# Kernel optimization log

Hardware: AMD Instinct MI355X
Metric: run time of the kernel (lower is better)

Reference implementation:

```python
import jax, jax.numpy as jnp
import numpy as np

N_NODES = 50000
N_EDGES = 800000
N_GRAPHS = 128
IN, HID, OUT, CLS = 128, 128, 128, 10


def setup_inputs() -> dict:
    key = jax.random.key(0)
    ks = jax.random.split(key, 16)
    d = {}
    d["features"] = jax.random.normal(ks[0], (N_NODES, IN), jnp.float32)
    d["edge_src"] = jax.random.randint(ks[1], (N_EDGES,), 0, N_NODES)
    d["edge_dst"] = jax.random.randint(ks[2], (N_EDGES,), 0, N_NODES)
    d["graph_ids"] = jnp.sort(jax.random.randint(ks[3], (N_NODES,), 0, N_GRAPHS))

    def lin(k, i, o):
        return (jax.random.normal(k, (i, o), jnp.float32) / np.float32(np.sqrt(i)))

    dims = [(IN, HID), (HID, HID), (HID, OUT)]
    for l, (i, o) in enumerate(dims):
        d[f"Ws{l}"] = lin(ks[4 + 3 * l], i, o)
        d[f"Wn{l}"] = lin(ks[5 + 3 * l], i, o)
        d[f"b{l}"] = jnp.zeros((o,), jnp.float32)
    d["Wf"] = lin(ks[13], OUT, CLS)
    d["bf"] = jnp.zeros((CLS,), jnp.float32)
    return d


def _sage_mean_layer(h, edge_src, edge_dst, Ws, Wn, b, in_deg):
    # mean-aggregate in-neighbor features: gather at src, segment-sum at dst
    msg_sum = jax.ops.segment_sum(h[edge_src], edge_dst, num_segments=N_NODES)
    h_neigh = msg_sum / in_deg  # [N, d], zero-degree nodes divide by 1 -> 0
    return jax.nn.relu(h @ Ws + h_neigh @ Wn + b)


def reference(features, edge_src, edge_dst, graph_ids,
              Ws0, Wn0, b0, Ws1, Wn1, b1, Ws2, Wn2, b2, Wf, bf):
    ones = jnp.ones((N_EDGES,), jnp.float32)
    in_deg = jax.ops.segment_sum(ones, edge_dst, num_segments=N_NODES)
    in_deg = jnp.maximum(in_deg, 1.0)[:, None]  # [N, 1]

    h = features
    h = _sage_mean_layer(h, edge_src, edge_dst, Ws0, Wn0, b0, in_deg)
    h = _sage_mean_layer(h, edge_src, edge_dst, Ws1, Wn1, b1, in_deg)
    h = _sage_mean_layer(h, edge_src, edge_dst, Ws2, Wn2, b2, in_deg)

    # mean graph pooling over node segments
    node_ones = jnp.ones((N_NODES,), jnp.float32)
    counts = jax.ops.segment_sum(node_ones, graph_ids, num_segments=N_GRAPHS)
    counts = jnp.maximum(counts, 1.0)[:, None]
    pooled = jax.ops.segment_sum(h, graph_ids, num_segments=N_GRAPHS) / counts

    return pooled @ Wf + bf  # [N_GRAPHS, CLS]
```

## Files before the change

### kernel.cpp

```cpp
#include <hip/hip_runtime.h>

#define N_NODES  50000
#define N_EDGES  800000
#define N_GRAPHS 128
#define HD       128
#define K2       256
#define CLS      10
#define NPART    8
#define PSIZE    (N_NODES / NPART)
#define NSUB     16
#define NB_SCAN  ((N_NODES + 255) / 256)
#define NBIN     1600
#define CHUNK    (N_EDGES / NBIN)
#define PCAP     131072
#define NSLOT    16

typedef __attribute__((ext_vector_type(8))) _Float16 f16x8;
typedef __attribute__((ext_vector_type(4))) float f32x4;
typedef __attribute__((ext_vector_type(2))) float f32x2;

union U4H8 { uint4 u; _Float16 h[8]; };
union U2H4 { uint2 u; _Float16 h[4]; };

typedef const __attribute__((address_space(1))) void* gptr_t;
typedef __attribute__((address_space(3))) void* lptr_t;
#define GLOAD_LDS16(g, l) \
    __builtin_amdgcn_global_load_lds((gptr_t)(g), (lptr_t)(l), 16, 0, 0)

__global__ __launch_bounds__(512) void k_zero(int* __restrict__ z) {
    int i = threadIdx.x;
    if (i < 264) z[i] = 0;
}

__global__ __launch_bounds__(256) void k_bin(const int* __restrict__ src, const int* __restrict__ dst,
                                             unsigned* __restrict__ stag, int* __restrict__ gcount) {
    __shared__ int lcount[NPART];
    __shared__ int lbase[NPART];
    const int tid = threadIdx.x;
    const int lo = blockIdx.x * CHUNK;
    if (tid < NPART) lcount[tid] = 0;
    __syncthreads();
    int dc[2], sc[2];
#pragma unroll
    for (int it = 0; it < 2; ++it) {
        int i = lo + tid + it * 256;
        dc[it] = -1;
        if (i < lo + CHUNK) {
            int d = dst[i];
            dc[it] = d; sc[it] = src[i];
            atomicAdd(&lcount[d / PSIZE], 1);
        }
    }
    __syncthreads();
    if (tid < NPART) {
        lbase[tid] = atomicAdd(&gcount[tid], lcount[tid]);
        lcount[tid] = 0;
    }
    __syncthreads();
#pragma unroll
    for (int it = 0; it < 2; ++it) {
        if (dc[it] >= 0) {
            int p = dc[it] / PSIZE;
            int slot = atomicAdd(&lcount[p], 1);
            stag[(size_t)p * PCAP + lbase[p] + slot] =
                (unsigned)sc[it] | ((unsigned)(dc[it] - p * PSIZE) << 16);
        }
    }
}

__global__ __launch_bounds__(512) void k_hist(const unsigned* __restrict__ stag,
                                              const int* __restrict__ gcount,
                                              int* __restrict__ ghist) {
    __shared__ int hist[PSIZE];
    const int tid = threadIdx.x;
    const int p = blockIdx.x & (NPART - 1);
    const int s = blockIdx.x >> 3;
    for (int j = tid; j < PSIZE; j += 512) hist[j] = 0;
    __syncthreads();
    const int n = gcount[p];
    const int cs = (int)(((long long)s * n) / NSUB);
    const int ce = (int)(((long long)(s + 1) * n) / NSUB);
    const unsigned* sp = stag + (size_t)p * PCAP;
    for (int i = cs + tid; i < ce; i += 512)
        atomicAdd(&hist[sp[i] >> 16], 1);
    __syncthreads();
    int* gh = ghist + (size_t)blockIdx.x * PSIZE;
    for (int j = tid; j < PSIZE; j += 512) gh[j] = hist[j];
}

__global__ __launch_bounds__(256) void k_scan(int* __restrict__ ghist,
                                              int* __restrict__ rowptr,
                                              int* __restrict__ bsum, int* __restrict__ bflag) {
    __shared__ int sc[256];
    __shared__ int r[256];
    const int tid = threadIdx.x;
    const int b = blockIdx.x;
    const int node = b * 256 + tid;
    int d[NSUB];
    int deg = 0, p = 0, off = 0;
    if (node < N_NODES) {
        p = node / PSIZE; off = node - p * PSIZE;
#pragma unroll
        for (int s = 0; s < NSUB; ++s) {
            d[s] = ghist[(size_t)(s * NPART + p) * PSIZE + off];
            deg += d[s];
        }
    }
    sc[tid] = deg;
    __syncthreads();
    for (int o = 1; o < 256; o <<= 1) {
        int add = (tid >= o) ? sc[tid - o] : 0;
        __syncthreads();
        sc[tid] += add;
        __syncthreads();
    }
    if (tid == 255) {
        __hip_atomic_store(&bsum[b], sc[255], __ATOMIC_RELAXED, __HIP_MEMORY_SCOPE_AGENT);
        __hip_atomic_store(&bflag[b], 1, __ATOMIC_RELEASE, __HIP_MEMORY_SCOPE_AGENT);
    }
    int agg = 0;
    if (tid < b) {
        while (__hip_atomic_load(&bflag[tid], __ATOMIC_ACQUIRE, __HIP_MEMORY_SCOPE_AGENT) == 0) {}
        agg = __hip_atomic_load(&bsum[tid], __ATOMIC_RELAXED, __HIP_MEMORY_SCOPE_AGENT);
    }
    r[tid] = agg;
    __syncthreads();
    for (int o = 128; o > 0; o >>= 1) {
        if (tid < o) r[tid] += r[tid + o];
        __syncthreads();
    }
    if (node < N_NODES) {
        int base = r[0] + sc[tid] - deg;
        rowptr[node] = base;
        int c = base;
#pragma unroll
        for (int s = 0; s < NSUB; ++s) {
            ghist[(size_t)(s * NPART + p) * PSIZE + off] = c;
            c += d[s];
        }
    }
    if (b == NB_SCAN - 1 && tid == 0) rowptr[N_NODES] = N_EDGES;
}

#define INIT_ITEMS (800000 + 3 * HD * K2 + N_GRAPHS * HD + N_GRAPHS)
#define INIT_BLOCKS5 ((INIT_ITEMS + 511) / 512)
__global__ __launch_bounds__(512) void k_scatterinit(
    const unsigned* __restrict__ stag, const int* __restrict__ gcount,
    const int* __restrict__ ghist, int* __restrict__ eidx,
    const float* __restrict__ f, unsigned short* __restrict__ c0, unsigned char* __restrict__ f8,
    const float* __restrict__ Ws0, const float* __restrict__ Wn0,
    const float* __restrict__ Ws1, const float* __restrict__ Wn1,
    const float* __restrict__ Ws2, const float* __restrict__ Wn2,
    unsigned short* __restrict__ wt, float* __restrict__ pooled,
    const int* __restrict__ gid, float* __restrict__ counts) {
    if (blockIdx.x < 128) {
        __shared__ int cur[PSIZE];
        const int tid = threadIdx.x;
        const int p = blockIdx.x & (NPART - 1);
        const int s = blockIdx.x >> 3;
        const int* gh = ghist + (size_t)blockIdx.x * PSIZE;
        for (int j = tid; j < PSIZE; j += 512) cur[j] = gh[j];
        __syncthreads();
        const int n = gcount[p];
        const int cs = (int)(((long long)s * n) / NSUB);
        const int ce = (int)(((long long)(s + 1) * n) / NSUB);
        const unsigned* sp = stag + (size_t)p * PCAP;
        for (int i = cs + tid; i < ce; i += 512) {
            unsigned v = sp[i];
            int slot = atomicAdd(&cur[v >> 16], 1);
            eidx[slot] = (int)(v & 0xFFFFu);
        }
        return;
    }
    long long gi = (long long)(blockIdx.x - 128) * 512 + threadIdx.x;
    if (gi < 800000) {
        int t = (int)gi;
        int row = t >> 4, c8 = (t & 15) * 8;
        const float* p = f + (size_t)row * HD + c8;
        float4 a = *(const float4*)p;
        float4 b = *(const float4*)(p + 4);
        U4H8 v;
        v.h[0] = (_Float16)a.x; v.h[1] = (_Float16)a.y;
        v.h[2] = (_Float16)a.z; v.h[3] = (_Float16)a.w;
        v.h[4] = (_Float16)b.x; v.h[5] = (_Float16)b.y;
        v.h[6] = (_Float16)b.z; v.h[7] = (_Float16)b.w;
        *(uint4*)(c0 + (size_t)row * K2 + c8) = v.u;
        int p0 = __builtin_amdgcn_cvt_pk_fp8_f32(a.x, a.y, 0, false);
        p0 = __builtin_amdgcn_cvt_pk_fp8_f32(a.z, a.w, p0, true);
        int p1 = __builtin_amdgcn_cvt_pk_fp8_f32(b.x, b.y, 0, false);
        p1 = __builtin_amdgcn_cvt_pk_fp8_f32(b.z, b.w, p1, true);
        *(uint2*)(f8 + (size_t)row * HD + c8) = make_uint2((unsigned)p0, (unsigned)p1);
        return;
    }
    gi -= 800000;
    if (gi < 3 * HD * K2) {
        int t = (int)gi;
        int l = t / (HD * K2), r = t % (HD * K2);
        int n = r / K2, k = r % K2;
        const float* Ws = (l == 0) ? Ws0 : (l == 1) ? Ws1 : Ws2;
        const float* Wn = (l == 0) ? Wn0 : (l == 1) ? Wn1 : Wn2;
        float w = (k < HD) ? Ws[k * HD + n] : Wn[(k - HD) * HD + n];
        union { unsigned short u; _Float16 h; } c;
        c.h = (_Float16)w;
        wt[t] = c.u;
        return;
    }
    gi -= 3 * HD * K2;
    if (gi < N_GRAPHS * HD) { pooled[gi] = 0.f; return; }
    gi -= (long long)N_GRAPHS * HD;
    if (gi < N_GRAPHS) {
        int g = (int)gi;
        int lo = 0, hi = N_NODES;
        while (lo < hi) { int mid = (lo + hi) >> 1; if (gid[mid] < g) lo = mid + 1; else hi = mid; }
        int start = lo;
        lo = 0; hi = N_NODES;
        while (lo < hi) { int mid = (lo + hi) >> 1; if (gid[mid] <= g) lo = mid + 1; else hi = mid; }
        counts[g] = (float)(lo - start);
    }
}

__global__ __launch_bounds__(256) void k_gather(const unsigned char* __restrict__ h8,
                                                const int* __restrict__ rowptr,
                                                const int* __restrict__ eidx,
                                                unsigned short* __restrict__ msg) {
    const int node = (blockIdx.x * 256 + threadIdx.x) >> 6;
    const int lane = threadIdx.x & 63;
    if (node >= N_NODES) return;
    const int epar = lane >> 4;
    const int d0 = (lane & 15) * 8;
    const int beg = rowptr[node], end = rowptr[node + 1];
    float acc[8] = {0.f, 0.f, 0.f, 0.f, 0.f, 0.f, 0.f, 0.f};
    int j = beg + epar;
    for (; j + 12 < end; j += 16) {
        int s0 = eidx[j], s1 = eidx[j + 4], s2 = eidx[j + 8], s3 = eidx[j + 12];
        uint2 v0 = *(const uint2*)(h8 + (size_t)s0 * HD + d0);
        uint2 v1 = *(const uint2*)(h8 + (size_t)s1 * HD + d0);
        uint2 v2 = *(const uint2*)(h8 + (size_t)s2 * HD + d0);
        uint2 v3 = *(const uint2*)(h8 + (size_t)s3 * HD + d0);
        f32x2 e;
        e = __builtin_amdgcn_cvt_pk_f32_fp8(v0.x, false); acc[0] += e[0]; acc[1] += e[1];
        e = __builtin_amdgcn_cvt_pk_f32_fp8(v0.x, true);  acc[2] += e[0]; acc[3] += e[1];
        e = __builtin_amdgcn_cvt_pk_f32_fp8(v0.y, false); acc[4] += e[0]; acc[5] += e[1];
        e = __builtin_amdgcn_cvt_pk_f32_fp8(v0.y, true);  acc[6] += e[0]; acc[7] += e[1];
        e = __builtin_amdgcn_cvt_pk_f32_fp8(v1.x, false); acc[0] += e[0]; acc[1] += e[1];
        e = __builtin_amdgcn_cvt_pk_f32_fp8(v1.x, true);  acc[2] += e[0]; acc[3] += e[1];
        e = __builtin_amdgcn_cvt_pk_f32_fp8(v1.y, false); acc[4] += e[0]; acc[5] += e[1];
        e = __builtin_amdgcn_cvt_pk_f32_fp8(v1.y, true);  acc[6] += e[0]; acc[7] += e[1];
        e = __builtin_amdgcn_cvt_pk_f32_fp8(v2.x, false); acc[0] += e[0]; acc[1] += e[1];
        e = __builtin_amdgcn_cvt_pk_f32_fp8(v2.x, true);  acc[2] += e[0]; acc[3] += e[1];
        e = __builtin_amdgcn_cvt_pk_f32_fp8(v2.y, false); acc[4] += e[0]; acc[5] += e[1];
        e = __builtin_amdgcn_cvt_pk_f32_fp8(v2.y, true);  acc[6] += e[0]; acc[7] += e[1];
        e = __builtin_amdgcn_cvt_pk_f32_fp8(v3.x, false); acc[0] += e[0]; acc[1] += e[1];
        e = __builtin_amdgcn_cvt_pk_f32_fp8(v3.x, true);  acc[2] += e[0]; acc[3] += e[1];
        e = __builtin_amdgcn_cvt_pk_f32_fp8(v3.y, false); acc[4] += e[0]; acc[5] += e[1];
        e = __builtin_amdgcn_cvt_pk_f32_fp8(v3.y, true);  acc[6] += e[0]; acc[7] += e[1];
    }
    for (; j < end; j += 4) {
        uint2 v0 = *(const uint2*)(h8 + (size_t)eidx[j] * HD + d0);
        f32x2 e;
        e = __builtin_amdgcn_cvt_pk_f32_fp8(v0.x, false); acc[0] += e[0]; acc[1] += e[1];
        e = __builtin_amdgcn_cvt_pk_f32_fp8(v0.x, true);  acc[2] += e[0]; acc[3] += e[1];
        e = __builtin_amdgcn_cvt_pk_f32_fp8(v0.y, false); acc[4] += e[0]; acc[5] += e[1];
        e = __builtin_amdgcn_cvt_pk_f32_fp8(v0.y, true);  acc[6] += e[0]; acc[7] += e[1];
    }
#pragma unroll
    for (int i = 0; i < 8; ++i) {
        acc[i] += __shfl_xor(acc[i], 16);
        acc[i] += __shfl_xor(acc[i], 32);
    }
    if (epar == 0) {
        float inv = (end > beg) ? 1.0f / (float)(end - beg) : 0.f;
        U4H8 o;
#pragma unroll
        for (int i = 0; i < 8; ++i) o.h[i] = (_Float16)(acc[i] * inv);
        *(uint4*)(msg + (size_t)node * K2 + HD + d0) = o.u;
    }
}

__global__ __launch_bounds__(256) void k_sage(const unsigned short* __restrict__ hin,
                                              const unsigned short* __restrict__ wt,
                                              const float* __restrict__ bias,
                                              unsigned short* __restrict__ hout,
                                              unsigned char* __restrict__ hout8,
                                              const int* __restrict__ gid,
                                              float* __restrict__ pooled,
                                              int write16, int dopool) {
    __shared__ __align__(16) _Float16 Ah[2][128 * 64];
    __shared__ __align__(16) _Float16 Bw[2][128 * 64];
    __shared__ float gpool[NSLOT][HD];
    __shared__ int ginfo[2];
    const int tid = threadIdx.x;
    const int wv = tid >> 6, lane = tid & 63;
    const int m0 = blockIdx.x * 128;
    const int m_off = (wv >> 1) * 64, n_off = (wv & 1) * 64;
    const int l15 = lane & 15, q = lane >> 4;

    f32x4 acc[4][4];
#pragma unroll
    for (int a = 0; a < 4; ++a)
#pragma unroll
        for (int b = 0; b < 4; ++b) acc[a][b] = (f32x4){0.f, 0.f, 0.f, 0.f};

    auto stage = [&](int bsel, int kt) {
        const int k0 = kt * 64;
#pragma unroll
        for (int i = 0; i < 4; ++i) {
            int idx = tid + i * 256;
            int row = idx >> 3, c = idx & 7;
            int qs = (c ^ (row & 7)) * 8;
            int gm = m0 + row;
            if (gm < N_NODES)
                GLOAD_LDS16(hin + (size_t)gm * K2 + k0 + qs, &Ah[bsel][idx * 8]);
            GLOAD_LDS16(wt + (size_t)row * K2 + k0 + qs, &Bw[bsel][idx * 8]);
        }
    };

    stage(0, 0);
    __syncthreads();
#pragma unroll
    for (int kt = 0; kt < 4; ++kt) {
        const int b = kt & 1;
        if (kt < 3) stage(b ^ 1, kt + 1);
        f16x8 hf[4][2], wf[4][2];
#pragma unroll
        for (int mt = 0; mt < 4; ++mt) {
            const int row = m_off + mt * 16 + l15;
            const int sw = row & 7;
#pragma unroll
            for (int ks = 0; ks < 2; ++ks)
                hf[mt][ks] = *(const f16x8*)&Ah[b][row * 64 + (((ks * 4 + q) ^ sw) * 8)];
        }
#pragma unroll
        for (int nt = 0; nt < 4; ++nt) {
            const int row = n_off + nt * 16 + l15;
            const int sw = row & 7;
#pragma unroll
            for (int ks = 0; ks < 2; ++ks)
                wf[nt][ks] = *(const f16x8*)&Bw[b][row * 64 + (((ks * 4 + q) ^ sw) * 8)];
        }
#pragma unroll
        for (int mt = 0; mt < 4; ++mt)
#pragma unroll
            for (int nt = 0; nt < 4; ++nt) {
                acc[mt][nt] = __builtin_amdgcn_mfma_f32_16x16x32_f16(wf[nt][0], hf[mt][0], acc[mt][nt], 0, 0, 0);
                acc[mt][nt] = __builtin_amdgcn_mfma_f32_16x16x32_f16(wf[nt][1], hf[mt][1], acc[mt][nt], 0, 0, 0);
            }
        __syncthreads();
    }
    if (!dopool) {
#pragma unroll
        for (int nt = 0; nt < 4; ++nt) {
            int n = n_off + nt * 16 + q * 4;
            float4 bv = *(const float4*)(bias + n);
#pragma unroll
            for (int mt = 0; mt < 4; ++mt) {
                int m = m0 + m_off + mt * 16 + l15;
                if (m < N_NODES) {
                    f32x4 a = acc[mt][nt];
                    float r0 = fmaxf(a[0] + bv.x, 0.f);
                    float r1 = fmaxf(a[1] + bv.y, 0.f);
                    float r2 = fmaxf(a[2] + bv.z, 0.f);
                    float r3 = fmaxf(a[3] + bv.w, 0.f);
                    if (write16) {
                        U2H4 v;
                        v.h[0] = (_Float16)r0; v.h[1] = (_Float16)r1;
                        v.h[2] = (_Float16)r2; v.h[3] = (_Float16)r3;
                        *(uint2*)(hout + (size_t)m * K2 + n) = v.u;
                    }
                    int p = __builtin_amdgcn_cvt_pk_fp8_f32(r0, r1, 0, false);
                    p = __builtin_amdgcn_cvt_pk_fp8_f32(r2, r3, p, true);
                    *(unsigned int*)(hout8 + (size_t)m * HD + n) = (unsigned)p;
                }
            }
        }
    } else {
        for (int j = tid; j < NSLOT * HD; j += 256) ((float*)gpool)[j] = 0.f;
        if (tid == 0) {
            ginfo[0] = gid[m0];
            ginfo[1] = gid[min(m0 + 127, N_NODES - 1)];
        }
        __syncthreads();
        const int g_lo = ginfo[0];
        int gg[4];
#pragma unroll
        for (int mt = 0; mt < 4; ++mt) {
            int m = m0 + m_off + mt * 16 + l15;
            gg[mt] = (m < N_NODES) ? gid[m] : -1;
        }
#pragma unroll
        for (int nt = 0; nt < 4; ++nt) {
            int n = n_off + nt * 16 + q * 4;
            float4 bv = *(const float4*)(bias + n);
            int cur = -1;
            float p0 = 0.f, p1 = 0.f, p2 = 0.f, p3 = 0.f;
#pragma unroll
            for (int mt = 0; mt < 4; ++mt) {
                if (gg[mt] < 0) continue;
                f32x4 a = acc[mt][nt];
                float r0 = fmaxf(a[0] + bv.x, 0.f);
                float r1 = fmaxf(a[1] + bv.y, 0.f);
                float r2 = fmaxf(a[2] + bv.z, 0.f);
                float r3 = fmaxf(a[3] + bv.w, 0.f);
                if (gg[mt] != cur) {
                    if (cur >= 0) {
                        int s = cur - g_lo;
                        if (s < NSLOT) {
                            atomicAdd(&gpool[s][n], p0); atomicAdd(&gpool[s][n + 1], p1);
                            atomicAdd(&gpool[s][n + 2], p2); atomicAdd(&gpool[s][n + 3], p3);
                        } else {
                            atomicAdd(&pooled[(size_t)cur * HD + n], p0);
                            atomicAdd(&pooled[(size_t)cur * HD + n + 1], p1);
                            atomicAdd(&pooled[(size_t)cur * HD + n + 2], p2);
                            atomicAdd(&pooled[(size_t)cur * HD + n + 3], p3);
                        }
                    }
                    cur = gg[mt]; p0 = r0; p1 = r1; p2 = r2; p3 = r3;
                } else {
                    p0 += r0; p1 += r1; p2 += r2; p3 += r3;
                }
            }
            if (cur >= 0) {
                int s = cur - g_lo;
                if (s < NSLOT) {
                    atomicAdd(&gpool[s][n], p0); atomicAdd(&gpool[s][n + 1], p1);
                    atomicAdd(&gpool[s][n + 2], p2); atomicAdd(&gpool[s][n + 3], p3);
                } else {
                    atomicAdd(&pooled[(size_t)cur * HD + n], p0);
                    atomicAdd(&pooled[(size_t)cur * HD + n + 1], p1);
                    atomicAdd(&pooled[(size_t)cur * HD + n + 2], p2);
                    atomicAdd(&pooled[(size_t)cur * HD + n + 3], p3);
                }
            }
        }
        __syncthreads();
        const int nslot = min(NSLOT, ginfo[1] - g_lo + 1);
        for (int j = tid; j < nslot * HD; j += 256) {
            float v = gpool[j >> 7][j & 127];
            if (v != 0.f)
                atomicAdd(&pooled[(size_t)(g_lo + (j >> 7)) * HD + (j & 127)], v);
        }
    }
}

__global__ __launch_bounds__(256) void k_final(const float* __restrict__ pooled,
                                               const float* __restrict__ counts,
                                               const float* __restrict__ Wf,
                                               const float* __restrict__ bf,
                                               float* __restrict__ out) {
    int t = blockIdx.x * 256 + threadIdx.x;
    if (t >= N_GRAPHS * CLS) return;
    int g = t / CLS, c = t % CLS;
    float inv = 1.0f / fmaxf(counts[g], 1.0f);
    float s = 0.f;
    for (int k = 0; k < HD; ++k) s += pooled[(size_t)g * HD + k] * Wf[k * CLS + c];
    out[t] = s * inv + bf[c];
}

extern "C" void kernel_launch(void* const* d_in, const int* in_sizes, int n_in,
                              void* d_out, int out_size, void* d_ws, size_t ws_size,
                              hipStream_t stream) {
    const float* features = (const float*)d_in[0];
    const int*   esrc     = (const int*)d_in[1];
    const int*   edst     = (const int*)d_in[2];
    const int*   gids     = (const int*)d_in[3];
    const float* bs[3]  = {(const float*)d_in[6], (const float*)d_in[9], (const float*)d_in[12]};
    const float* Wf = (const float*)d_in[13];
    const float* bfv = (const float*)d_in[14];
    float* out = (float*)d_out;

    int* gcount = (int*)d_ws;
    int* bflag  = gcount + 8;
    int* bsum   = bflag + 256;
    int* rowptr = bsum + 256;
    int* eidx   = rowptr + 50008;
    unsigned* stag = (unsigned*)(eidx + 800000);
    int* ghist  = (int*)(stag + (size_t)NPART * PCAP);
    float* pooled = (float*)(ghist + (size_t)NPART * NSUB * PSIZE);
    float* counts = pooled + N_GRAPHS * HD;
    unsigned short* C0 = (unsigned short*)(counts + 128);
    unsigned short* C1 = C0 + (size_t)N_NODES * K2;
    unsigned short* C2 = C1 + (size_t)N_NODES * K2;
    unsigned short* Wt = C2 + (size_t)N_NODES * K2;
    unsigned char* F0 = (unsigned char*)(Wt + 3 * HD * K2);
    unsigned char* F1 = F0 + (size_t)N_NODES * HD;
    unsigned char* F2 = F1 + (size_t)N_NODES * HD;

    k_zero<<<1, 512, 0, stream>>>(gcount);

    k_bin<<<NBIN, 256, 0, stream>>>(esrc, edst, stag, gcount);
    k_hist<<<NPART * NSUB, 512, 0, stream>>>(stag, gcount, ghist);
    k_scan<<<NB_SCAN, 256, 0, stream>>>(ghist, rowptr, bsum, bflag);
    k_scatterinit<<<128 + INIT_BLOCKS5, 512, 0, stream>>>(
        stag, gcount, ghist, eidx,
        features, C0, F0,
        (const float*)d_in[4], (const float*)d_in[5],
        (const float*)d_in[7], (const float*)d_in[8],
        (const float*)d_in[10], (const float*)d_in[11],
        Wt, pooled, gids, counts);

    unsigned short* C[4] = {C0, C1, C2, C0};
    unsigned char* F[4] = {F0, F1, F2, F0};
    for (int l = 0; l < 3; ++l) {
        k_gather<<<(N_NODES * 64 + 255) / 256, 256, 0, stream>>>(F[l], rowptr, eidx, C[l]);
        k_sage<<<(N_NODES + 127) / 128, 256, 0, stream>>>(
            C[l], Wt + (size_t)l * HD * K2, bs[l], C[l + 1], F[l + 1],
            gids, pooled, (l < 2) ? 1 : 0, (l == 2) ? 1 : 0);
    }

    k_final<<<(N_GRAPHS * CLS + 255) / 256, 256, 0, stream>>>(pooled, counts, Wf, bfv, out);
}
```

Before: 291.5 us.

## Fuse neighbor gather into SAGE GEMM kernel with LDS-resident messages

Merges the per-layer gather kernel and the GEMM kernel into one 512-thread kernel. Each block first aggregates the mean neighbor messages for its 128 nodes into shared memory, then runs the MFMA GEMM reading the self half from global and the neighbor half from LDS. This removes the global write and re-read of the message half of the concatenated buffer and one launch per layer, and it narrows the activation buffers to 128 columns. In exchange the gather parallelism per block is serialized over 16 nodes per wave, double buffering is replaced by single-buffer staging with extra barriers, and LDS use grows, which may lower occupancy.

```diff
diff --git a/kernel.cpp b/kernel.cpp
--- a/kernel.cpp
+++ b/kernel.cpp
@@ -184,7 +184,7 @@
         v.h[2] = (_Float16)a.z; v.h[3] = (_Float16)a.w;
         v.h[4] = (_Float16)b.x; v.h[5] = (_Float16)b.y;
         v.h[6] = (_Float16)b.z; v.h[7] = (_Float16)b.w;
-        *(uint4*)(c0 + (size_t)row * K2 + c8) = v.u;
+        *(uint4*)(c0 + (size_t)row * HD + c8) = v.u;
         int p0 = __builtin_amdgcn_cvt_pk_fp8_f32(a.x, a.y, 0, false);
         p0 = __builtin_amdgcn_cvt_pk_fp8_f32(a.z, a.w, p0, true);
         int p1 = __builtin_amdgcn_cvt_pk_fp8_f32(b.x, b.y, 0, false);
@@ -219,116 +219,130 @@
     }
 }
 
-__global__ __launch_bounds__(256) void k_gather(const unsigned char* __restrict__ h8,
-                                                const int* __restrict__ rowptr,
-                                                const int* __restrict__ eidx,
-                                                unsigned short* __restrict__ msg) {
-    const int node = (blockIdx.x * 256 + threadIdx.x) >> 6;
-    const int lane = threadIdx.x & 63;
-    if (node >= N_NODES) return;
-    const int epar = lane >> 4;
-    const int d0 = (lane & 15) * 8;
-    const int beg = rowptr[node], end = rowptr[node + 1];
-    float acc[8] = {0.f, 0.f, 0.f, 0.f, 0.f, 0.f, 0.f, 0.f};
-    int j = beg + epar;
-    for (; j + 12 < end; j += 16) {
-        int s0 = eidx[j], s1 = eidx[j + 4], s2 = eidx[j + 8], s3 = eidx[j + 12];
-        uint2 v0 = *(const uint2*)(h8 + (size_t)s0 * HD + d0);
-        uint2 v1 = *(const uint2*)(h8 + (size_t)s1 * HD + d0);
-        uint2 v2 = *(const uint2*)(h8 + (size_t)s2 * HD + d0);
-        uint2 v3 = *(const uint2*)(h8 + (size_t)s3 * HD + d0);
-        f32x2 e;
-        e = __builtin_amdgcn_cvt_pk_f32_fp8(v0.x, false); acc[0] += e[0]; acc[1] += e[1];
-        e = __builtin_amdgcn_cvt_pk_f32_fp8(v0.x, true);  acc[2] += e[0]; acc[3] += e[1];
-        e = __builtin_amdgcn_cvt_pk_f32_fp8(v0.y, false); acc[4] += e[0]; acc[5] += e[1];
-        e = __builtin_amdgcn_cvt_pk_f32_fp8(v0.y, true);  acc[6] += e[0]; acc[7] += e[1];
-        e = __builtin_amdgcn_cvt_pk_f32_fp8(v1.x, false); acc[0] += e[0]; acc[1] += e[1];
-        e = __builtin_amdgcn_cvt_pk_f32_fp8(v1.x, true);  acc[2] += e[0]; acc[3] += e[1];
-        e = __builtin_amdgcn_cvt_pk_f32_fp8(v1.y, false); acc[4] += e[0]; acc[5] += e[1];
-        e = __builtin_amdgcn_cvt_pk_f32_fp8(v1.y, true);  acc[6] += e[0]; acc[7] += e[1];
-        e = __builtin_amdgcn_cvt_pk_f32_fp8(v2.x, false); acc[0] += e[0]; acc[1] += e[1];
-        e = __builtin_amdgcn_cvt_pk_f32_fp8(v2.x, true);  acc[2] += e[0]; acc[3] += e[1];
-        e = __builtin_amdgcn_cvt_pk_f32_fp8(v2.y, false); acc[4] += e[0]; acc[5] += e[1];
-        e = __builtin_amdgcn_cvt_pk_f32_fp8(v2.y, true);  acc[6] += e[0]; acc[7] += e[1];
-        e = __builtin_amdgcn_cvt_pk_f32_fp8(v3.x, false); acc[0] += e[0]; acc[1] += e[1];
-        e = __builtin_amdgcn_cvt_pk_f32_fp8(v3.x, true);  acc[2] += e[0]; acc[3] += e[1];
-        e = __builtin_amdgcn_cvt_pk_f32_fp8(v3.y, false); acc[4] += e[0]; acc[5] += e[1];
-        e = __builtin_amdgcn_cvt_pk_f32_fp8(v3.y, true);  acc[6] += e[0]; acc[7] += e[1];
-    }
-    for (; j < end; j += 4) {
-        uint2 v0 = *(const uint2*)(h8 + (size_t)eidx[j] * HD + d0);
-        f32x2 e;
-        e = __builtin_amdgcn_cvt_pk_f32_fp8(v0.x, false); acc[0] += e[0]; acc[1] += e[1];
-        e = __builtin_amdgcn_cvt_pk_f32_fp8(v0.x, true);  acc[2] += e[0]; acc[3] += e[1];
-        e = __builtin_amdgcn_cvt_pk_f32_fp8(v0.y, false); acc[4] += e[0]; acc[5] += e[1];
-        e = __builtin_amdgcn_cvt_pk_f32_fp8(v0.y, true);  acc[6] += e[0]; acc[7] += e[1];
-    }
-#pragma unroll
-    for (int i = 0; i < 8; ++i) {
-        acc[i] += __shfl_xor(acc[i], 16);
-        acc[i] += __shfl_xor(acc[i], 32);
-    }
-    if (epar == 0) {
-        float inv = (end > beg) ? 1.0f / (float)(end - beg) : 0.f;
-        U4H8 o;
-#pragma unroll
-        for (int i = 0; i < 8; ++i) o.h[i] = (_Float16)(acc[i] * inv);
-        *(uint4*)(msg + (size_t)node * K2 + HD + d0) = o.u;
-    }
-}
-
-__global__ __launch_bounds__(256) void k_sage(const unsigned short* __restrict__ hin,
-                                              const unsigned short* __restrict__ wt,
-                                              const float* __restrict__ bias,
-                                              unsigned short* __restrict__ hout,
-                                              unsigned char* __restrict__ hout8,
-                                              const int* __restrict__ gid,
-                                              float* __restrict__ pooled,
-                                              int write16, int dopool) {
-    __shared__ __align__(16) _Float16 Ah[2][128 * 64];
-    __shared__ __align__(16) _Float16 Bw[2][128 * 64];
-    __shared__ float gpool[NSLOT][HD];
+__global__ __launch_bounds__(512) void k_gsage(const unsigned char* __restrict__ h8,
+                                               const unsigned short* __restrict__ hin,
+                                               const int* __restrict__ rowptr,
+                                               const int* __restrict__ eidx,
+                                               const unsigned short* __restrict__ wt,
+                                               const float* __restrict__ bias,
+                                               unsigned short* __restrict__ hout,
+                                               unsigned char* __restrict__ hout8,
+                                               const int* __restrict__ gid,
+                                               float* __restrict__ pooled,
+                                               int dopool) {
+    __shared__ __align__(16) char arena[65536];
+    _Float16* Ah  = (_Float16*)arena;
+    _Float16* Bw  = (_Float16*)(arena + 16384);
+    _Float16* msg = (_Float16*)(arena + 32768);
+    float (*gpool)[HD] = (float(*)[HD])arena;
     __shared__ int ginfo[2];
     const int tid = threadIdx.x;
     const int wv = tid >> 6, lane = tid & 63;
     const int m0 = blockIdx.x * 128;
-    const int m_off = (wv >> 1) * 64, n_off = (wv & 1) * 64;
+    const int m_off = (wv >> 1) * 32, n_off = (wv & 1) * 64;
     const int l15 = lane & 15, q = lane >> 4;
 
-    f32x4 acc[4][4];
-#pragma unroll
-    for (int a = 0; a < 4; ++a)
-#pragma unroll
-        for (int b = 0; b < 4; ++b) acc[a][b] = (f32x4){0.f, 0.f, 0.f, 0.f};
-
-    auto stage = [&](int bsel, int kt) {
+    auto stageA = [&](int kt) {
         const int k0 = kt * 64;
 #pragma unroll
-        for (int i = 0; i < 4; ++i) {
-            int idx = tid + i * 256;
+        for (int i = 0; i < 2; ++i) {
+            int idx = tid + i * 512;
             int row = idx >> 3, c = idx & 7;
             int qs = (c ^ (row & 7)) * 8;
             int gm = m0 + row;
             if (gm < N_NODES)
-                GLOAD_LDS16(hin + (size_t)gm * K2 + k0 + qs, &Ah[bsel][idx * 8]);
-            GLOAD_LDS16(wt + (size_t)row * K2 + k0 + qs, &Bw[bsel][idx * 8]);
+                GLOAD_LDS16(hin + (size_t)gm * HD + k0 + qs, &Ah[idx * 8]);
         }
     };
-
-    stage(0, 0);
-    __syncthreads();
+    auto stageB = [&](int kt) {
+        const int k0 = kt * 64;
+#pragma unroll
+        for (int i = 0; i < 2; ++i) {
+            int idx = tid + i * 512;
+            int row = idx >> 3, c = idx & 7;
+            int qs = (c ^ (row & 7)) * 8;
+            GLOAD_LDS16(wt + (size_t)row * K2 + k0 + qs, &Bw[idx * 8]);
+        }
+    };
+
+    stageA(0); stageB(0);
+
+    const int epar = lane >> 4;
+    const int d0 = l15 * 8;
+    for (int i = 0; i < 16; ++i) {
+        const int r = wv * 16 + i;
+        const int node = m0 + r;
+        if (node >= N_NODES) break;
+        const int beg = rowptr[node], end = rowptr[node + 1];
+        float acc[8] = {0.f, 0.f, 0.f, 0.f, 0.f, 0.f, 0.f, 0.f};
+        int j = beg + epar;
+        for (; j + 12 < end; j += 16) {
+            int s0 = eidx[j], s1 = eidx[j + 4], s2 = eidx[j + 8], s3 = eidx[j + 12];
+            uint2 v0 = *(const uint2*)(h8 + (size_t)s0 * HD + d0);
+            uint2 v1 = *(const uint2*)(h8 + (size_t)s1 * HD + d0);
+            uint2 v2 = *(const uint2*)(h8 + (size_t)s2 * HD + d0);
+            uint2 v3 = *(const uint2*)(h8 + (size_t)s3 * HD + d0);
+            f32x2 e;
+            e = __builtin_amdgcn_cvt_pk_f32_fp8(v0.x, false); acc[0] += e[0]; acc[1] += e[1];
+            e = __builtin_amdgcn_cvt_pk_f32_fp8(v0.x, true);  acc[2] += e[0]; acc[3] += e[1];
+            e = __builtin_amdgcn_cvt_pk_f32_fp8(v0.y, false); acc[4] += e[0]; acc[5] += e[1];
+            e = __builtin_amdgcn_cvt_pk_f32_fp8(v0.y, true);  acc[6] += e[0]; acc[7] += e[1];
+            e = __builtin_amdgcn_cvt_pk_f32_fp8(v1.x, false); acc[0] += e[0]; acc[1] += e[1];
+            e = __builtin_amdgcn_cvt_pk_f32_fp8(v1.x, true);  acc[2] += e[0]; acc[3] += e[1];
+            e = __builtin_amdgcn_cvt_pk_f32_fp8(v1.y, false); acc[4] += e[0]; acc[5] += e[1];
+            e = __builtin_amdgcn_cvt_pk_f32_fp8(v1.y, true);  acc[6] += e[0]; acc[7] += e[1];
+            e = __builtin_amdgcn_cvt_pk_f32_fp8(v2.x, false); acc[0] += e[0]; acc[1] += e[1];
+            e = __builtin_amdgcn_cvt_pk_f32_fp8(v2.x, true);  acc[2] += e[0]; acc[3] += e[1];
+            e = __builtin_amdgcn_cvt_pk_f32_fp8(v2.y, false); acc[4] += e[0]; acc[5] += e[1];
+            e = __builtin_amdgcn_cvt_pk_f32_fp8(v2.y, true);  acc[6] += e[0]; acc[7] += e[1];
+            e = __builtin_amdgcn_cvt_pk_f32_fp8(v3.x, false); acc[0] += e[0]; acc[1] += e[1];
+            e = __builtin_amdgcn_cvt_pk_f32_fp8(v3.x, true);  acc[2] += e[0]; acc[3] += e[1];
+            e = __builtin_amdgcn_cvt_pk_f32_fp8(v3.y, false); acc[4] += e[0]; acc[5] += e[1];
+            e = __builtin_amdgcn_cvt_pk_f32_fp8(v3.y, true);  acc[6] += e[0]; acc[7] += e[1];
+        }
+        for (; j < end; j += 4) {
+            uint2 v0 = *(const uint2*)(h8 + (size_t)eidx[j] * HD + d0);
+            f32x2 e;
+            e = __builtin_amdgcn_cvt_pk_f32_fp8(v0.x, false); acc[0] += e[0]; acc[1] += e[1];
+            e = __builtin_amdgcn_cvt_pk_f32_fp8(v0.x, true);  acc[2] += e[0]; acc[3] += e[1];
+            e = __builtin_amdgcn_cvt_pk_f32_fp8(v0.y, false); acc[4] += e[0]; acc[5] += e[1];
+            e = __builtin_amdgcn_cvt_pk_f32_fp8(v0.y, true);  acc[6] += e[0]; acc[7] += e[1];
+        }
+#pragma unroll
+        for (int k = 0; k < 8; ++k) {
+            acc[k] += __shfl_xor(acc[k], 16);
+            acc[k] += __shfl_xor(acc[k], 32);
+        }
+        if (epar == 0) {
+            float inv = (end > beg) ? 1.0f / (float)(end - beg) : 0.f;
+            U4H8 o;
+#pragma unroll
+            for (int k = 0; k < 8; ++k) o.h[k] = (_Float16)(acc[k] * inv);
+            *(uint4*)&msg[(size_t)r * 128 + ((l15 ^ (r & 7)) * 8)] = o.u;
+        }
+    }
+    __syncthreads();
+
+    f32x4 acc[2][4];
+#pragma unroll
+    for (int a = 0; a < 2; ++a)
+#pragma unroll
+        for (int b = 0; b < 4; ++b) acc[a][b] = (f32x4){0.f, 0.f, 0.f, 0.f};
+
 #pragma unroll
     for (int kt = 0; kt < 4; ++kt) {
-        const int b = kt & 1;
-        if (kt < 3) stage(b ^ 1, kt + 1);
-        f16x8 hf[4][2], wf[4][2];
-#pragma unroll
-        for (int mt = 0; mt < 4; ++mt) {
+        f16x8 hf[2][2], wf[4][2];
+#pragma unroll
+        for (int mt = 0; mt < 2; ++mt) {
             const int row = m_off + mt * 16 + l15;
             const int sw = row & 7;
 #pragma unroll
-            for (int ks = 0; ks < 2; ++ks)
-                hf[mt][ks] = *(const f16x8*)&Ah[b][row * 64 + (((ks * 4 + q) ^ sw) * 8)];
+            for (int ks = 0; ks < 2; ++ks) {
+                if (kt < 2)
+                    hf[mt][ks] = *(const f16x8*)&Ah[row * 64 + (((ks * 4 + q) ^ sw) * 8)];
+                else
+                    hf[mt][ks] = *(const f16x8*)&msg[row * 128 + ((((kt - 2) * 8 + ks * 4 + q) ^ sw) * 8)];
+            }
         }
 #pragma unroll
         for (int nt = 0; nt < 4; ++nt) {
@@ -336,10 +350,15 @@
             const int sw = row & 7;
 #pragma unroll
             for (int ks = 0; ks < 2; ++ks)
-                wf[nt][ks] = *(const f16x8*)&Bw[b][row * 64 + (((ks * 4 + q) ^ sw) * 8)];
-        }
-#pragma unroll
-        for (int mt = 0; mt < 4; ++mt)
+                wf[nt][ks] = *(const f16x8*)&Bw[row * 64 + (((ks * 4 + q) ^ sw) * 8)];
+        }
+        __syncthreads();
+        if (kt < 3) {
+            if (kt == 0) stageA(1);
+            stageB(kt + 1);
+        }
+#pragma unroll
+        for (int mt = 0; mt < 2; ++mt)
 #pragma unroll
             for (int nt = 0; nt < 4; ++nt) {
                 acc[mt][nt] = __builtin_amdgcn_mfma_f32_16x16x32_f16(wf[nt][0], hf[mt][0], acc[mt][nt], 0, 0, 0);
@@ -347,13 +366,14 @@
             }
         __syncthreads();
     }
+
     if (!dopool) {
 #pragma unroll
         for (int nt = 0; nt < 4; ++nt) {
             int n = n_off + nt * 16 + q * 4;
             float4 bv = *(const float4*)(bias + n);
 #pragma unroll
-            for (int mt = 0; mt < 4; ++mt) {
+            for (int mt = 0; mt < 2; ++mt) {
                 int m = m0 + m_off + mt * 16 + l15;
                 if (m < N_NODES) {
                     f32x4 a = acc[mt][nt];
@@ -361,12 +381,10 @@
                     float r1 = fmaxf(a[1] + bv.y, 0.f);
                     float r2 = fmaxf(a[2] + bv.z, 0.f);
                     float r3 = fmaxf(a[3] + bv.w, 0.f);
-                    if (write16) {
-                        U2H4 v;
-                        v.h[0] = (_Float16)r0; v.h[1] = (_Float16)r1;
-                        v.h[2] = (_Float16)r2; v.h[3] = (_Float16)r3;
-                        *(uint2*)(hout + (size_t)m * K2 + n) = v.u;
-                    }
+                    U2H4 v;
+                    v.h[0] = (_Float16)r0; v.h[1] = (_Float16)r1;
+                    v.h[2] = (_Float16)r2; v.h[3] = (_Float16)r3;
+                    *(uint2*)(hout + (size_t)m * HD + n) = v.u;
                     int p = __builtin_amdgcn_cvt_pk_fp8_f32(r0, r1, 0, false);
                     p = __builtin_amdgcn_cvt_pk_fp8_f32(r2, r3, p, true);
                     *(unsigned int*)(hout8 + (size_t)m * HD + n) = (unsigned)p;
@@ -374,16 +392,16 @@
             }
         }
     } else {
-        for (int j = tid; j < NSLOT * HD; j += 256) ((float*)gpool)[j] = 0.f;
+        for (int j = tid; j < NSLOT * HD; j += 512) ((float*)gpool)[j] = 0.f;
         if (tid == 0) {
             ginfo[0] = gid[m0];
             ginfo[1] = gid[min(m0 + 127, N_NODES - 1)];
         }
         __syncthreads();
         const int g_lo = ginfo[0];
-        int gg[4];
-#pragma unroll
-        for (int mt = 0; mt < 4; ++mt) {
+        int gg[2];
+#pragma unroll
+        for (int mt = 0; mt < 2; ++mt) {
             int m = m0 + m_off + mt * 16 + l15;
             gg[mt] = (m < N_NODES) ? gid[m] : -1;
         }
@@ -394,7 +412,7 @@
             int cur = -1;
             float p0 = 0.f, p1 = 0.f, p2 = 0.f, p3 = 0.f;
 #pragma unroll
-            for (int mt = 0; mt < 4; ++mt) {
+            for (int mt = 0; mt < 2; ++mt) {
                 if (gg[mt] < 0) continue;
                 f32x4 a = acc[mt][nt];
                 float r0 = fmaxf(a[0] + bv.x, 0.f);
@@ -434,7 +452,7 @@
         }
         __syncthreads();
         const int nslot = min(NSLOT, ginfo[1] - g_lo + 1);
-        for (int j = tid; j < nslot * HD; j += 256) {
+        for (int j = tid; j < nslot * HD; j += 512) {
             float v = gpool[j >> 7][j & 127];
             if (v != 0.f)
                 atomicAdd(&pooled[(size_t)(g_lo + (j >> 7)) * HD + (j & 127)], v);
@@ -478,9 +496,9 @@
     float* pooled = (float*)(ghist + (size_t)NPART * NSUB * PSIZE);
     float* counts = pooled + N_GRAPHS * HD;
     unsigned short* C0 = (unsigned short*)(counts + 128);
-    unsigned short* C1 = C0 + (size_t)N_NODES * K2;
-    unsigned short* C2 = C1 + (size_t)N_NODES * K2;
-    unsigned short* Wt = C2 + (size_t)N_NODES * K2;
+    unsigned short* C1 = C0 + (size_t)N_NODES * HD;
+    unsigned short* C2 = C1 + (size_t)N_NODES * HD;
+    unsigned short* Wt = C2 + (size_t)N_NODES * HD;
     unsigned char* F0 = (unsigned char*)(Wt + 3 * HD * K2);
     unsigned char* F1 = F0 + (size_t)N_NODES * HD;
     unsigned char* F2 = F1 + (size_t)N_NODES * HD;
@@ -501,10 +519,9 @@
     unsigned short* C[4] = {C0, C1, C2, C0};
     unsigned char* F[4] = {F0, F1, F2, F0};
     for (int l = 0; l < 3; ++l) {
-        k_gather<<<(N_NODES * 64 + 255) / 256, 256, 0, stream>>>(F[l], rowptr, eidx, C[l]);
-        k_sage<<<(N_NODES + 127) / 128, 256, 0, stream>>>(
-            C[l], Wt + (size_t)l * HD * K2, bs[l], C[l + 1], F[l + 1],
-            gids, pooled, (l < 2) ? 1 : 0, (l == 2) ? 1 : 0);
+        k_gsage<<<(N_NODES + 127) / 128, 512, 0, stream>>>(
+            F[l], C[l], rowptr, eidx, Wt + (size_t)l * HD * K2, bs[l],
+            C[l + 1], F[l + 1], gids, pooled, (l == 2) ? 1 : 0);
     }
 
     k_final<<<(N_GRAPHS * CLS + 255) / 256, 256, 0, stream>>>(pooled, counts, Wf, bfv, out);
```

Result: slower. 353.3 us (+21.2%).

## Fuse histogram, scan and scatter into one kernel with software grid barriers

Applied to the files above, without the earlier changes.

Merges the histogram, prefix-scan and scatter kernels into a single k_build kernel. Its first 128 worker blocks synchronise through atomic-counter grid barriers, while the remaining blocks do the feature, weight and pooling initialisation. This removes two kernel launches and their inter-kernel gaps. It relies on all 128 worker blocks being co-resident; if they are not, the spin barriers can deadlock, and the extra init blocks may compete with workers for occupancy.

```diff
diff --git a/kernel.cpp b/kernel.cpp
--- a/kernel.cpp
+++ b/kernel.cpp
@@ -9,11 +9,12 @@
 #define NPART    8
 #define PSIZE    (N_NODES / NPART)
 #define NSUB     16
-#define NB_SCAN  ((N_NODES + 255) / 256)
 #define NBIN     1600
 #define CHUNK    (N_EDGES / NBIN)
 #define PCAP     131072
 #define NSLOT    16
+#define NWRK     128
+#define NPB      391
 
 typedef __attribute__((ext_vector_type(8))) _Float16 f16x8;
 typedef __attribute__((ext_vector_type(4))) float f32x4;
@@ -27,9 +28,18 @@
 #define GLOAD_LDS16(g, l) \
     __builtin_amdgcn_global_load_lds((gptr_t)(g), (lptr_t)(l), 16, 0, 0)
 
-__global__ __launch_bounds__(512) void k_zero(int* __restrict__ z) {
-    int i = threadIdx.x;
-    if (i < 264) z[i] = 0;
+__device__ __forceinline__ void gbar(int* cnt) {
+    __threadfence();
+    __syncthreads();
+    if (threadIdx.x == 0) {
+        __hip_atomic_fetch_add(cnt, 1, __ATOMIC_ACQ_REL, __HIP_MEMORY_SCOPE_AGENT);
+        while (__hip_atomic_load(cnt, __ATOMIC_ACQUIRE, __HIP_MEMORY_SCOPE_AGENT) < NWRK) {}
+    }
+    __syncthreads();
+}
+
+__global__ __launch_bounds__(64) void k_zero(int* __restrict__ z) {
+    if (threadIdx.x < 16) z[threadIdx.x] = 0;
 }
 
 __global__ __launch_bounds__(256) void k_bin(const int* __restrict__ src, const int* __restrict__ dst,
@@ -68,154 +78,147 @@
     }
 }
 
-__global__ __launch_bounds__(512) void k_hist(const unsigned* __restrict__ stag,
-                                              const int* __restrict__ gcount,
-                                              int* __restrict__ ghist) {
-    __shared__ int hist[PSIZE];
-    const int tid = threadIdx.x;
-    const int p = blockIdx.x & (NPART - 1);
-    const int s = blockIdx.x >> 3;
-    for (int j = tid; j < PSIZE; j += 512) hist[j] = 0;
-    __syncthreads();
-    const int n = gcount[p];
-    const int cs = (int)(((long long)s * n) / NSUB);
-    const int ce = (int)(((long long)(s + 1) * n) / NSUB);
-    const unsigned* sp = stag + (size_t)p * PCAP;
-    for (int i = cs + tid; i < ce; i += 512)
-        atomicAdd(&hist[sp[i] >> 16], 1);
-    __syncthreads();
-    int* gh = ghist + (size_t)blockIdx.x * PSIZE;
-    for (int j = tid; j < PSIZE; j += 512) gh[j] = hist[j];
-}
-
-__global__ __launch_bounds__(256) void k_scan(int* __restrict__ ghist,
-                                              int* __restrict__ rowptr,
-                                              int* __restrict__ bsum, int* __restrict__ bflag) {
-    __shared__ int sc[256];
-    __shared__ int r[256];
-    const int tid = threadIdx.x;
-    const int b = blockIdx.x;
-    const int node = b * 256 + tid;
-    int d[NSUB];
-    int deg = 0, p = 0, off = 0;
-    if (node < N_NODES) {
-        p = node / PSIZE; off = node - p * PSIZE;
-#pragma unroll
-        for (int s = 0; s < NSUB; ++s) {
-            d[s] = ghist[(size_t)(s * NPART + p) * PSIZE + off];
-            deg += d[s];
-        }
-    }
-    sc[tid] = deg;
-    __syncthreads();
-    for (int o = 1; o < 256; o <<= 1) {
-        int add = (tid >= o) ? sc[tid - o] : 0;
-        __syncthreads();
-        sc[tid] += add;
-        __syncthreads();
-    }
-    if (tid == 255) {
-        __hip_atomic_store(&bsum[b], sc[255], __ATOMIC_RELAXED, __HIP_MEMORY_SCOPE_AGENT);
-        __hip_atomic_store(&bflag[b], 1, __ATOMIC_RELEASE, __HIP_MEMORY_SCOPE_AGENT);
-    }
-    int agg = 0;
-    if (tid < b) {
-        while (__hip_atomic_load(&bflag[tid], __ATOMIC_ACQUIRE, __HIP_MEMORY_SCOPE_AGENT) == 0) {}
-        agg = __hip_atomic_load(&bsum[tid], __ATOMIC_RELAXED, __HIP_MEMORY_SCOPE_AGENT);
-    }
-    r[tid] = agg;
-    __syncthreads();
-    for (int o = 128; o > 0; o >>= 1) {
-        if (tid < o) r[tid] += r[tid + o];
-        __syncthreads();
-    }
-    if (node < N_NODES) {
-        int base = r[0] + sc[tid] - deg;
-        rowptr[node] = base;
-        int c = base;
-#pragma unroll
-        for (int s = 0; s < NSUB; ++s) {
-            ghist[(size_t)(s * NPART + p) * PSIZE + off] = c;
-            c += d[s];
-        }
-    }
-    if (b == NB_SCAN - 1 && tid == 0) rowptr[N_NODES] = N_EDGES;
-}
-
 #define INIT_ITEMS (800000 + 3 * HD * K2 + N_GRAPHS * HD + N_GRAPHS)
 #define INIT_BLOCKS5 ((INIT_ITEMS + 511) / 512)
-__global__ __launch_bounds__(512) void k_scatterinit(
+__global__ __launch_bounds__(512) void k_build(
     const unsigned* __restrict__ stag, const int* __restrict__ gcount,
-    const int* __restrict__ ghist, int* __restrict__ eidx,
+    int* __restrict__ ghist, int* __restrict__ rowptr, int* __restrict__ eidx,
+    int* __restrict__ bsum, int* __restrict__ cnts,
     const float* __restrict__ f, unsigned short* __restrict__ c0, unsigned char* __restrict__ f8,
     const float* __restrict__ Ws0, const float* __restrict__ Wn0,
     const float* __restrict__ Ws1, const float* __restrict__ Wn1,
     const float* __restrict__ Ws2, const float* __restrict__ Wn2,
     unsigned short* __restrict__ wt, float* __restrict__ pooled,
     const int* __restrict__ gid, float* __restrict__ counts) {
-    if (blockIdx.x < 128) {
-        __shared__ int cur[PSIZE];
-        const int tid = threadIdx.x;
-        const int p = blockIdx.x & (NPART - 1);
-        const int s = blockIdx.x >> 3;
-        const int* gh = ghist + (size_t)blockIdx.x * PSIZE;
-        for (int j = tid; j < PSIZE; j += 512) cur[j] = gh[j];
-        __syncthreads();
-        const int n = gcount[p];
-        const int cs = (int)(((long long)s * n) / NSUB);
-        const int ce = (int)(((long long)(s + 1) * n) / NSUB);
-        const unsigned* sp = stag + (size_t)p * PCAP;
+    const int tid = threadIdx.x;
+    const int blk = blockIdx.x;
+    if (blk >= NWRK) {
+        long long gi = (long long)(blk - NWRK) * 512 + tid;
+        if (gi < 800000) {
+            int t = (int)gi;
+            int row = t >> 4, c8 = (t & 15) * 8;
+            const float* p = f + (size_t)row * HD + c8;
+            float4 a = *(const float4*)p;
+            float4 b = *(const float4*)(p + 4);
+            U4H8 v;
+            v.h[0] = (_Float16)a.x; v.h[1] = (_Float16)a.y;
+            v.h[2] = (_Float16)a.z; v.h[3] = (_Float16)a.w;
+            v.h[4] = (_Float16)b.x; v.h[5] = (_Float16)b.y;
+            v.h[6] = (_Float16)b.z; v.h[7] = (_Float16)b.w;
+            *(uint4*)(c0 + (size_t)row * K2 + c8) = v.u;
+            int p0 = __builtin_amdgcn_cvt_pk_fp8_f32(a.x, a.y, 0, false);
+            p0 = __builtin_amdgcn_cvt_pk_fp8_f32(a.z, a.w, p0, true);
+            int p1 = __builtin_amdgcn_cvt_pk_fp8_f32(b.x, b.y, 0, false);
+            p1 = __builtin_amdgcn_cvt_pk_fp8_f32(b.z, b.w, p1, true);
+            *(uint2*)(f8 + (size_t)row * HD + c8) = make_uint2((unsigned)p0, (unsigned)p1);
+            return;
+        }
+        gi -= 800000;
+        if (gi < 3 * HD * K2) {
+            int t = (int)gi;
+            int l = t / (HD * K2), r = t % (HD * K2);
+            int n = r / K2, k = r % K2;
+            const float* Ws = (l == 0) ? Ws0 : (l == 1) ? Ws1 : Ws2;
+            const float* Wn = (l == 0) ? Wn0 : (l == 1) ? Wn1 : Wn2;
+            float w = (k < HD) ? Ws[k * HD + n] : Wn[(k - HD) * HD + n];
+            union { unsigned short u; _Float16 h; } c;
+            c.h = (_Float16)w;
+            wt[t] = c.u;
+            return;
+        }
+        gi -= 3 * HD * K2;
+        if (gi < N_GRAPHS * HD) { pooled[gi] = 0.f; return; }
+        gi -= (long long)N_GRAPHS * HD;
+        if (gi < N_GRAPHS) {
+            int g = (int)gi;
+            int lo = 0, hi = N_NODES;
+            while (lo < hi) { int mid = (lo + hi) >> 1; if (gid[mid] < g) lo = mid + 1; else hi = mid; }
+            int start = lo;
+            lo = 0; hi = N_NODES;
+            while (lo < hi) { int mid = (lo + hi) >> 1; if (gid[mid] <= g) lo = mid + 1; else hi = mid; }
+            counts[g] = (float)(lo - start);
+        }
+        return;
+    }
+    __shared__ int hist[PSIZE];
+    __shared__ int s512[512];
+    const int p = blk & (NPART - 1);
+    const int s = blk >> 3;
+    const int n = gcount[p];
+    const int cs = (int)(((long long)s * n) / NSUB);
+    const int ce = (int)(((long long)(s + 1) * n) / NSUB);
+    const unsigned* sp = stag + (size_t)p * PCAP;
+
+    for (int j = tid; j < PSIZE; j += 512) hist[j] = 0;
+    __syncthreads();
+    for (int i = cs + tid; i < ce; i += 512)
+        atomicAdd(&hist[sp[i] >> 16], 1);
+    __syncthreads();
+    {
+        int* gh = ghist + (size_t)blk * PSIZE;
+        for (int j = tid; j < PSIZE; j += 512) gh[j] = hist[j];
+    }
+    gbar(&cnts[0]);
+
+    const int node = blk * NPB + tid;
+    int d[NSUB];
+    int deg = 0, pn = 0, off = 0;
+    if (tid < NPB && node < N_NODES) {
+        pn = node / PSIZE; off = node - pn * PSIZE;
+#pragma unroll
+        for (int q = 0; q < NSUB; ++q) {
+            d[q] = ghist[(size_t)(q * NPART + pn) * PSIZE + off];
+            deg += d[q];
+        }
+    }
+    s512[tid] = deg;
+    __syncthreads();
+    for (int o = 1; o < 512; o <<= 1) {
+        int add = (tid >= o) ? s512[tid - o] : 0;
+        __syncthreads();
+        s512[tid] += add;
+        __syncthreads();
+    }
+    const int lex = s512[tid] - deg;
+    if (tid == 511) bsum[blk] = s512[511];
+    gbar(&cnts[1]);
+
+    if (blk == 0) {
+        int v = (tid < NWRK) ? bsum[tid] : 0;
+        s512[tid] = v;
+        __syncthreads();
+        for (int o = 1; o < 512; o <<= 1) {
+            int add = (tid >= o) ? s512[tid - o] : 0;
+            __syncthreads();
+            s512[tid] += add;
+            __syncthreads();
+        }
+        if (tid < NWRK) bsum[tid] = s512[tid] - v;
+    }
+    gbar(&cnts[2]);
+
+    if (tid < NPB && node < N_NODES) {
+        int base = bsum[blk] + lex;
+        rowptr[node] = base;
+        int c = base;
+#pragma unroll
+        for (int q = 0; q < NSUB; ++q) {
+            ghist[(size_t)(q * NPART + pn) * PSIZE + off] = c;
+            c += d[q];
+        }
+    }
+    if (blk == 0 && tid == 0) rowptr[N_NODES] = N_EDGES;
+    gbar(&cnts[3]);
+
+    {
+        const int* gh = ghist + (size_t)blk * PSIZE;
+        for (int j = tid; j < PSIZE; j += 512) hist[j] = gh[j];
+        __syncthreads();
         for (int i = cs + tid; i < ce; i += 512) {
             unsigned v = sp[i];
-            int slot = atomicAdd(&cur[v >> 16], 1);
+            int slot = atomicAdd(&hist[v >> 16], 1);
             eidx[slot] = (int)(v & 0xFFFFu);
         }
-        return;
-    }
-    long long gi = (long long)(blockIdx.x - 128) * 512 + threadIdx.x;
-    if (gi < 800000) {
-        int t = (int)gi;
-        int row = t >> 4, c8 = (t & 15) * 8;
-        const float* p = f + (size_t)row * HD + c8;
-        float4 a = *(const float4*)p;
-        float4 b = *(const float4*)(p + 4);
-        U4H8 v;
-        v.h[0] = (_Float16)a.x; v.h[1] = (_Float16)a.y;
-        v.h[2] = (_Float16)a.z; v.h[3] = (_Float16)a.w;
-        v.h[4] = (_Float16)b.x; v.h[5] = (_Float16)b.y;
-        v.h[6] = (_Float16)b.z; v.h[7] = (_Float16)b.w;
-        *(uint4*)(c0 + (size_t)row * K2 + c8) = v.u;
-        int p0 = __builtin_amdgcn_cvt_pk_fp8_f32(a.x, a.y, 0, false);
-        p0 = __builtin_amdgcn_cvt_pk_fp8_f32(a.z, a.w, p0, true);
-        int p1 = __builtin_amdgcn_cvt_pk_fp8_f32(b.x, b.y, 0, false);
-        p1 = __builtin_amdgcn_cvt_pk_fp8_f32(b.z, b.w, p1, true);
-        *(uint2*)(f8 + (size_t)row * HD + c8) = make_uint2((unsigned)p0, (unsigned)p1);
-        return;
-    }
-    gi -= 800000;
-    if (gi < 3 * HD * K2) {
-        int t = (int)gi;
-        int l = t / (HD * K2), r = t % (HD * K2);
-        int n = r / K2, k = r % K2;
-        const float* Ws = (l == 0) ? Ws0 : (l == 1) ? Ws1 : Ws2;
-        const float* Wn = (l == 0) ? Wn0 : (l == 1) ? Wn1 : Wn2;
-        float w = (k < HD) ? Ws[k * HD + n] : Wn[(k - HD) * HD + n];
-        union { unsigned short u; _Float16 h; } c;
-        c.h = (_Float16)w;
-        wt[t] = c.u;
-        return;
-    }
-    gi -= 3 * HD * K2;
-    if (gi < N_GRAPHS * HD) { pooled[gi] = 0.f; return; }
-    gi -= (long long)N_GRAPHS * HD;
-    if (gi < N_GRAPHS) {
-        int g = (int)gi;
-        int lo = 0, hi = N_NODES;
-        while (lo < hi) { int mid = (lo + hi) >> 1; if (gid[mid] < g) lo = mid + 1; else hi = mid; }
-        int start = lo;
-        lo = 0; hi = N_NODES;
-        while (lo < hi) { int mid = (lo + hi) >> 1; if (gid[mid] <= g) lo = mid + 1; else hi = mid; }
-        counts[g] = (float)(lo - start);
     }
 }
 
@@ -469,8 +472,8 @@
     float* out = (float*)d_out;
 
     int* gcount = (int*)d_ws;
-    int* bflag  = gcount + 8;
-    int* bsum   = bflag + 256;
+    int* cnts   = gcount + 8;
+    int* bsum   = cnts + 8;
     int* rowptr = bsum + 256;
     int* eidx   = rowptr + 50008;
     unsigned* stag = (unsigned*)(eidx + 800000);
@@ -485,13 +488,12 @@
     unsigned char* F1 = F0 + (size_t)N_NODES * HD;
     unsigned char* F2 = F1 + (size_t)N_NODES * HD;
 
-    k_zero<<<1, 512, 0, stream>>>(gcount);
+    k_zero<<<1, 64, 0, stream>>>(gcount);
 
     k_bin<<<NBIN, 256, 0, stream>>>(esrc, edst, stag, gcount);
-    k_hist<<<NPART * NSUB, 512, 0, stream>>>(stag, gcount, ghist);
-    k_scan<<<NB_SCAN, 256, 0, stream>>>(ghist, rowptr, bsum, bflag);
-    k_scatterinit<<<128 + INIT_BLOCKS5, 512, 0, stream>>>(
-        stag, gcount, ghist, eidx,
+
+    k_build<<<NWRK + INIT_BLOCKS5, 512, 0, stream>>>(
+        stag, gcount, ghist, rowptr, eidx, bsum, cnts,
         features, C0, F0,
         (const float*)d_in[4], (const float*)d_in[5],
         (const float*)d_in[7], (const float*)d_in[8],
```

Result: slower. 383.3 us (+31.5%).
